# Performance work log

Hardware: AMD Instinct MI355X
Metric: run time of the kernel (lower is better)

The kernel has to match this reference:

```python
import jax, jax.numpy as jnp
import numpy as np

B, S, D = 2, 2048, 2048
NH, NKV, HD = 16, 4, 128  # num_heads, num_key_value_heads, head_dim

def setup_inputs() -> dict:
    key = jax.random.key(0)
    ks = jax.random.split(key, 5)
    sc = 0.02
    return {
        "hidden_states": jax.random.normal(ks[0], (B, S, D), jnp.float32),
        "Wq": jax.random.normal(ks[1], (NH * HD, D), jnp.float32) * sc,
        "Wk": jax.random.normal(ks[2], (NKV * HD, D), jnp.float32) * sc,
        "Wv": jax.random.normal(ks[3], (NKV * HD, D), jnp.float32) * sc,
        "Wo": jax.random.normal(ks[4], (D, NH * HD), jnp.float32) * sc,
    }

def reference(hidden_states, Wq, Wk, Wv, Wo):
    b, s, d = hidden_states.shape
    # projections (LLaMA linear: x @ W.T)
    q = jnp.einsum('bsd,ed->bse', hidden_states, Wq).reshape(b, s, NH, HD).transpose(0, 2, 1, 3)
    k = jnp.einsum('bsd,ed->bse', hidden_states, Wk).reshape(b, s, NKV, HD).transpose(0, 2, 1, 3)
    v = jnp.einsum('bsd,ed->bse', hidden_states, Wv).reshape(b, s, NKV, HD).transpose(0, 2, 1, 3)
    # GQA: repeat kv heads
    n_rep = NH // NKV
    k = jnp.repeat(k, n_rep, axis=1)  # [b, NH, s, HD]
    v = jnp.repeat(v, n_rep, axis=1)
    scale = 1.0 / jnp.sqrt(jnp.asarray(HD, hidden_states.dtype))
    scores = jnp.einsum('bhqd,bhkd->bhqk', q, k) * scale
    causal = jnp.tril(jnp.ones((s, s), bool))
    scores = jnp.where(causal, scores, jnp.asarray(-jnp.inf, scores.dtype))
    attn = jax.nn.softmax(scores, axis=-1)
    out = jnp.einsum('bhqk,bhkd->bhqd', attn, v)  # [b, NH, s, HD]
    out = out.transpose(0, 2, 1, 3).reshape(b, s, NH * HD)
    return jnp.einsum('bse,de->bsd', out, Wo)
```

## Files before the change

### kernel.cpp

```cpp
#include <hip/hip_runtime.h>

typedef unsigned short u16;
typedef unsigned int u32;
typedef __attribute__((ext_vector_type(4))) float f32x4;
typedef __attribute__((ext_vector_type(16))) float f32x16;
typedef __attribute__((ext_vector_type(8))) short bf16x8;


__device__ __forceinline__ u16 f2b(float f) {
  u32 u = __builtin_bit_cast(u32, f);
  u = (u + 0x7fffu + ((u >> 16) & 1u)) >> 16;
  return (u16)u;
}

__device__ __forceinline__ void gload_lds16(const void* g, void* l) {
  __builtin_amdgcn_global_load_lds((const __attribute__((address_space(1))) u32*)g,
                                   (__attribute__((address_space(3))) u32*)l, 16, 0, 0);
}

#if __has_builtin(__builtin_amdgcn_permlane32_swap)
#define HAS_PLS 1
__device__ __forceinline__ void pls(u32 x, u32 y, u32& rx, u32& ry) {
  auto r = __builtin_amdgcn_permlane32_swap(x, y, false, false);
  rx = (u32)r[0];
  ry = (u32)r[1];
}
#endif

__device__ __forceinline__ float xhalf_max(float v) {
#ifdef HAS_PLS
  u32 a, b;
  pls(__builtin_bit_cast(u32, v), __builtin_bit_cast(u32, v), a, b);
  return fmaxf(__builtin_bit_cast(float, a), __builtin_bit_cast(float, b));
#else
  return fmaxf(v, __shfl_xor(v, 32));
#endif
}

__device__ __forceinline__ float xhalf_sum(float v) {
#ifdef HAS_PLS
  u32 a, b;
  pls(__builtin_bit_cast(u32, v), __builtin_bit_cast(u32, v), a, b);
  return __builtin_bit_cast(float, a) + __builtin_bit_cast(float, b);
#else
  return v + __shfl_xor(v, 32);
#endif
}

__device__ __forceinline__ void xexchange(int hi, u32 a0, u32 a1, u32 a2, u32 a3, u32* o) {
#ifdef HAS_PLS
  pls(a0, a2, o[0], o[2]);
  pls(a1, a3, o[1], o[3]);
#else
  u32 xa0 = (u32)__shfl_xor((int)a0, 32), xa1 = (u32)__shfl_xor((int)a1, 32);
  u32 xa2 = (u32)__shfl_xor((int)a2, 32), xa3 = (u32)__shfl_xor((int)a3, 32);
  o[0] = hi ? xa2 : a0;
  o[1] = hi ? xa3 : a1;
  o[2] = hi ? a2 : xa0;
  o[3] = hi ? a3 : xa1;
#endif
}

__device__ __forceinline__ u32 pktrunc(float lo, float hif) {
  return (__builtin_bit_cast(u32, lo) >> 16) | (__builtin_bit_cast(u32, hif) & 0xffff0000u);
}

__global__ void cvt_bf16(const float* __restrict__ src, u16* __restrict__ dst, int n) {
  int stride = gridDim.x * blockDim.x * 4;
  for (int idx = (blockIdx.x * blockDim.x + threadIdx.x) * 4; idx < n; idx += stride) {
    float4 v = *(const float4*)(src + idx);
    ushort4 o;
    o.x = f2b(v.x); o.y = f2b(v.y); o.z = f2b(v.z); o.w = f2b(v.w);
    *(ushort4*)(dst + idx) = o;
  }
}

__global__ void cvt_w4(const float* __restrict__ Wq, const float* __restrict__ Wk,
                       const float* __restrict__ Wv, const float* __restrict__ Wo,
                       u16* __restrict__ dst) {
  const int total = 10485760;
  int stride = gridDim.x * blockDim.x * 4;
  for (int idx = (blockIdx.x * blockDim.x + threadIdx.x) * 4; idx < total; idx += stride) {
    const float* src;
    int off;
    if (idx < 4194304) { src = Wq; off = idx; }
    else if (idx < 5242880) { src = Wk; off = idx - 4194304; }
    else if (idx < 6291456) { src = Wv; off = idx - 5242880; }
    else { src = Wo; off = idx - 6291456; }
    float4 v = *(const float4*)(src + off);
    ushort4 o;
    o.x = f2b(v.x); o.y = f2b(v.y); o.z = f2b(v.z); o.w = f2b(v.w);
    *(ushort4*)(dst + idx) = o;
  }
}

template<int OUT_MODE>
__global__ __launch_bounds__(256) void gemm_bt(const u16* __restrict__ A, const u16* __restrict__ B,
                                               void* __restrict__ Cout, int M, int N, int Kd,
                                               u16* __restrict__ Kout, u16* __restrict__ Vtout) {
  __shared__ u16 smem[(OUT_MODE == 3) ? 16384 : 8192];
  u16* sA = smem;
  u16* sB = smem + 4096;
  const int tid = threadIdx.x;
  const int l = tid & 63, w = tid >> 6;
  const int wr = w >> 1, wc = w & 1;
  const int g = l >> 4, c = l & 15;
  const int tm = blockIdx.y * 128, tn = blockIdx.x * 128;

  f32x4 acc[4][4] = {};

  const int r0 = tid >> 2, cc = (tid & 3) << 3;

  for (int k0 = 0; k0 < Kd; k0 += 32) {
    __syncthreads();
    {
      const u16* srcA0 = A + (size_t)(tm + r0) * Kd + k0 + cc;
      const u16* srcB0 = B + (size_t)(tn + r0) * Kd + k0 + cc;
      gload_lds16(srcA0, (char*)sA + w * 1024);
      gload_lds16(srcB0, (char*)sB + w * 1024);
      gload_lds16(srcA0 + (size_t)64 * Kd, (char*)sA + 4096 + w * 1024);
      gload_lds16(srcB0 + (size_t)64 * Kd, (char*)sB + 4096 + w * 1024);
    }
    __syncthreads();

    bf16x8 af[4], bfr[4];
#pragma unroll
    for (int m = 0; m < 4; ++m)
      af[m] = *(const bf16x8*)(sA + (wr * 64 + m * 16 + c) * 32 + g * 8);
#pragma unroll
    for (int n = 0; n < 4; ++n)
      bfr[n] = *(const bf16x8*)(sB + (wc * 64 + n * 16 + c) * 32 + g * 8);
#pragma unroll
    for (int m = 0; m < 4; ++m)
#pragma unroll
      for (int n = 0; n < 4; ++n)
        acc[m][n] = __builtin_amdgcn_mfma_f32_16x16x32_bf16(af[m], bfr[n], acc[m][n], 0, 0, 0);
  }

  if constexpr (OUT_MODE == 3) {
    if (tn >= 2048) {
      const bool isK = tn < 2560;
      __syncthreads();
#pragma unroll
      for (int m = 0; m < 4; ++m)
#pragma unroll
        for (int n = 0; n < 4; ++n)
#pragma unroll
          for (int i = 0; i < 4; ++i) {
            int lr = wr * 64 + m * 16 + g * 4 + i;
            int lc = wc * 64 + n * 16 + c;
            int off;
            if (isK)
              off = ((lr >> 5) << 12) + ((lc >> 4) << 9) + (((lc >> 3) & 1) << 8) +
                    ((lr & 31) << 3) + (lc & 7);
            else
              off = ((lr >> 5) << 12) + (((lr >> 4) & 1) << 11) + ((lc >> 5) << 9) +
                    (((lr >> 3) & 1) << 8) + ((lc & 31) << 3) + (lr & 7);
            smem[off] = f2b(acc[m][n][i]);
          }
      __syncthreads();
      const int e0 = tn - (isK ? 2048 : 2560);
      const int bb = tm >> 11;
      u16* dstbase = (isK ? Kout : Vtout) +
                     ((((size_t)(bb * 4 + (e0 >> 7)) * 64 + ((tm & 2047) >> 5))) << 12);
#pragma unroll
      for (int ps = 0; ps < 8; ++ps) {
        int idx = ps * 2048 + tid * 8;
        *(bf16x8*)(dstbase + idx) = *(const bf16x8*)(smem + idx);
      }
      return;
    }
  }

#pragma unroll
  for (int m = 0; m < 4; ++m)
#pragma unroll
    for (int n = 0; n < 4; ++n)
#pragma unroll
      for (int i = 0; i < 4; ++i) {
        int row = tm + wr * 64 + m * 16 + g * 4 + i;
        int col = tn + wc * 64 + n * 16 + c;
        float v = acc[m][n][i];
        if constexpr (OUT_MODE == 2) {
          ((float*)Cout)[(size_t)row * N + col] = v;
        } else {
          ((u16*)Cout)[(size_t)row * 2048 + col] = f2b(v);
        }
      }
}

__global__ __launch_bounds__(256, 2) void attn_fwd(const u16* __restrict__ Q, const u16* __restrict__ Kf,
                                                   const u16* __restrict__ Vf, u16* __restrict__ AO) {
  const int l = threadIdx.x & 63, w = threadIdx.x >> 6;
  const int ql = l & 31, hi = l >> 5;
  const int bh = blockIdx.y;
  const int b = bh >> 4, h = bh & 15;
  const int kvh = h >> 2;

  __shared__ float4 mO[2][16][64];
  __shared__ float mML[2][2][64];

  const float sm = 0.08838834764831845f * 1.4426950408889634f;

  const u16* Kfb = Kf + (size_t)(b * 4 + kvh) * 64 * 4096 + l * 8;
  const u16* Vfb = Vf + (size_t)(b * 4 + kvh) * 64 * 4096 + l * 8;

  const int ti = w & 1, kvhalf = w >> 1;
  const int t = ti ? (63 - (int)blockIdx.x) : (int)blockIdx.x;
  const int q0 = t * 32;

  bf16x8 qf[8];
  {
    const u16* qb = Q + ((size_t)(b * 2048 + q0 + ql)) * 2048 + h * 128 + hi * 8;
#pragma unroll
    for (int ck = 0; ck < 8; ++ck) qf[ck] = *(const bf16x8*)(qb + ck * 16);
  }

  f32x16 acc[4] = {};
  float mrow = -1e30f, lrow = 0.f;

  bf16x8 kfa[8], kfb[8];

#define LOADK(KF, KV0)                                                        \
  do {                                                                        \
    const u16* kb_ = Kfb + (size_t)((KV0) >> 5) * 4096;                       \
    _Pragma("unroll") for (int ck = 0; ck < 8; ++ck)                          \
        KF[ck] = *(const bf16x8*)(kb_ + ck * 512);                            \
  } while (0)

#define COMPUTE(KF, KV0)                                                      \
  do {                                                                        \
    bf16x8 vtf[2][4];                                                         \
    {                                                                         \
      const u16* vb_ = Vfb + (size_t)((KV0) >> 5) * 4096;                     \
      _Pragma("unroll") for (int ks = 0; ks < 2; ++ks)                        \
      _Pragma("unroll") for (int db = 0; db < 4; ++db)                        \
          vtf[ks][db] = *(const bf16x8*)(vb_ + (ks * 4 + db) * 512);          \
    }                                                                         \
    f32x16 sacc = {};                                                         \
    __builtin_amdgcn_s_setprio(1);                                            \
    _Pragma("unroll") for (int ck = 0; ck < 8; ++ck)                          \
        sacc = __builtin_amdgcn_mfma_f32_32x32x16_bf16(KF[ck], qf[ck], sacc, 0, 0, 0); \
    __builtin_amdgcn_s_setprio(0);                                            \
    if ((KV0) == q0) {                             \
      _Pragma("unroll") for (int r = 0; r < 16; ++r) {                        \
        int crow = (r & 3) + 8 * (r >> 2) + 4 * hi;                           \
        if (crow > ql) sacc[r] = -1e30f;                                      \
      }                                                                       \
    }                                                                         \
    float t0 = fmaxf(sacc[0], sacc[1]), t1 = fmaxf(sacc[2], sacc[3]);         \
    float t2 = fmaxf(sacc[4], sacc[5]), t3 = fmaxf(sacc[6], sacc[7]);         \
    float t4 = fmaxf(sacc[8], sacc[9]), t5 = fmaxf(sacc[10], sacc[11]);       \
    float t6 = fmaxf(sacc[12], sacc[13]), t7 = fmaxf(sacc[14], sacc[15]);     \
    float mx = fmaxf(fmaxf(fmaxf(t0, t1), fmaxf(t2, t3)),                     \
                     fmaxf(fmaxf(t4, t5), fmaxf(t6, t7)));                    \
    mx = xhalf_max(mx);                                                       \
    float p[16];                                                              \
    _Pragma("unroll") for (int r = 0; r < 16; ++r)                            \
        p[r] = exp2f((sacc[r] - mrow) * sm);                                  \
    if (!__all((mx - mrow) * sm <= 8.0f)) {                \
      float mnew = fmaxf(mrow, mx);                                           \
      float rs = exp2f((mrow - mnew) * sm);                                   \
      mrow = mnew;                                                            \
      lrow *= rs;                                                             \
      _Pragma("unroll") for (int db = 0; db < 4; ++db)                        \
      _Pragma("unroll") for (int r = 0; r < 16; ++r) acc[db][r] *= rs;        \
      _Pragma("unroll") for (int r = 0; r < 16; ++r)                          \
          p[r] = exp2f((sacc[r] - mrow) * sm);                                \
    }                                                                         \
    float s0 = p[0] + p[1], s1 = p[2] + p[3], s2 = p[4] + p[5], s3 = p[6] + p[7]; \
    float s4 = p[8] + p[9], s5 = p[10] + p[11], s6 = p[12] + p[13], s7 = p[14] + p[15]; \
    float psum = ((s0 + s1) + (s2 + s3)) + ((s4 + s5) + (s6 + s7));           \
    lrow += xhalf_sum(psum);                                                  \
    u32 a0 = pktrunc(p[0], p[1]), a1 = pktrunc(p[2], p[3]);                   \
    u32 a2 = pktrunc(p[4], p[5]), a3 = pktrunc(p[6], p[7]);                   \
    u32 b0 = pktrunc(p[8], p[9]), b1 = pktrunc(p[10], p[11]);                 \
    u32 b2 = pktrunc(p[12], p[13]), b3 = pktrunc(p[14], p[15]);               \
    union { bf16x8 v; u32 u[4]; } pa0, pa1;                                   \
    xexchange(hi, a0, a1, a2, a3, pa0.u);                                     \
    xexchange(hi, b0, b1, b2, b3, pa1.u);                                     \
    __builtin_amdgcn_s_setprio(1);                                            \
    _Pragma("unroll") for (int db = 0; db < 4; ++db) {                        \
      acc[db] = __builtin_amdgcn_mfma_f32_32x32x16_bf16(vtf[0][db], pa0.v, acc[db], 0, 0, 0); \
      acc[db] = __builtin_amdgcn_mfma_f32_32x32x16_bf16(vtf[1][db], pa1.v, acc[db], 0, 0, 0); \
    }                                                                         \
    __builtin_amdgcn_s_setprio(0);                                            \
  } while (0)

  int kv0 = kvhalf * 32;
  if (kv0 <= q0) {
    LOADK(kfa, kv0);
    while (true) {
      bool more = kv0 + 64 <= q0;
      if (more) LOADK(kfb, kv0 + 64);
      COMPUTE(kfa, kv0);
      if (!more) break;
      kv0 += 64;
      more = kv0 + 64 <= q0;
      if (more) LOADK(kfa, kv0 + 64);
      COMPUTE(kfb, kv0);
      if (!more) break;
      kv0 += 64;
    }
  }
#undef LOADK
#undef COMPUTE

  if (kvhalf) {
#pragma unroll
    for (int db = 0; db < 4; ++db)
#pragma unroll
      for (int rq = 0; rq < 4; ++rq) {
        float4 v;
        v.x = acc[db][rq * 4 + 0];
        v.y = acc[db][rq * 4 + 1];
        v.z = acc[db][rq * 4 + 2];
        v.w = acc[db][rq * 4 + 3];
        mO[ti][db * 4 + rq][l] = v;
      }
    mML[ti][0][l] = mrow;
    mML[ti][1][l] = lrow;
  }
  __syncthreads();
  if (!kvhalf) {
    float m1 = mML[ti][0][l], l1 = mML[ti][1][l];
    float mnew = fmaxf(mrow, m1);
    float s0 = exp2f((mrow - mnew) * sm);
    float s1 = exp2f((m1 - mnew) * sm);
    float inv = 1.0f / (lrow * s0 + l1 * s1);
    float f0 = s0 * inv, f1 = s1 * inv;
    u16* ob = AO + (size_t)(b * 2048 + q0 + ql) * 2048 + h * 128 + hi * 4;
#pragma unroll
    for (int db = 0; db < 4; ++db)
#pragma unroll
      for (int rq = 0; rq < 4; ++rq) {
        float4 o1 = mO[ti][db * 4 + rq][l];
        ushort4 o;
        o.x = f2b(acc[db][rq * 4 + 0] * f0 + o1.x * f1);
        o.y = f2b(acc[db][rq * 4 + 1] * f0 + o1.y * f1);
        o.z = f2b(acc[db][rq * 4 + 2] * f0 + o1.z * f1);
        o.w = f2b(acc[db][rq * 4 + 3] * f0 + o1.w * f1);
        *(ushort4*)(ob + db * 32 + rq * 8) = o;
      }
  }
}

extern "C" void kernel_launch(void* const* d_in, const int* in_sizes, int n_in,
                              void* d_out, int out_size, void* d_ws, size_t ws_size,
                              hipStream_t stream) {
  const float* X = (const float*)d_in[0];
  const float* Wq = (const float*)d_in[1];
  const float* Wk = (const float*)d_in[2];
  const float* Wv = (const float*)d_in[3];
  const float* Wo = (const float*)d_in[4];

  u16* ws = (u16*)d_ws;
  const size_t nX = 8388608;
  const size_t nWq = 4194304;
  const size_t nWk = 1048576;
  u16* Xb = ws;
  u16* Wqb = Xb + nX;
  u16* Wkb = Wqb + nWq;
  u16* Wvb = Wkb + nWk;
  u16* Wob = Wvb + nWk;
  u16* Qb = Wob + nWq;
  u16* Kfb = Qb + nX;
  u16* Vfb = Kfb + 2097152;
  u16* AOb = Vfb + 2097152;
  if (ws_size < (size_t)(39845888) * 2) return;

  cvt_bf16<<<2048, 256, 0, stream>>>(X, Xb, (int)nX);
  cvt_w4<<<2048, 256, 0, stream>>>(Wq, Wk, Wv, Wo, Wqb);

  gemm_bt<3><<<dim3(24, 32), 256, 0, stream>>>(Xb, Wqb, Qb, 4096, 3072, 2048, Kfb, Vfb);

  attn_fwd<<<dim3(32, 32), 256, 0, stream>>>(Qb, Kfb, Vfb, AOb);

  gemm_bt<2><<<dim3(16, 32), 256, 0, stream>>>(AOb, Wob, d_out, 4096, 2048, 2048, nullptr, nullptr);
}
```

Before: 216.2 us.

## Split each query tile's KV range across four waves with tree merge

Each block now processes a single 32-row query tile, and its four waves stride over the KV range in steps of 128 instead of two waves handling paired mirrored tiles. Partial softmax states are combined through LDS in a two-step tree reduction, and the grid doubles with tiles launched heaviest-first. This shortens the per-wave serial KV loop and improves load balance. In exchange it adds extra barriers and merge work, and each block gets less work.

```diff
diff --git a/kernel.cpp b/kernel.cpp
--- a/kernel.cpp
+++ b/kernel.cpp
@@ -205,8 +205,7 @@
   const u16* Kfb = Kf + (size_t)(b * 4 + kvh) * 64 * 4096 + l * 8;
   const u16* Vfb = Vf + (size_t)(b * 4 + kvh) * 64 * 4096 + l * 8;
 
-  const int ti = w & 1, kvhalf = w >> 1;
-  const int t = ti ? (63 - (int)blockIdx.x) : (int)blockIdx.x;
+  const int t = 63 - (int)blockIdx.x;
   const int q0 = t * 32;
 
   bf16x8 qf[8];
@@ -287,62 +286,82 @@
     __builtin_amdgcn_s_setprio(0);                                            \
   } while (0)
 
-  int kv0 = kvhalf * 32;
+  int kv0 = w * 32;
   if (kv0 <= q0) {
     LOADK(kfa, kv0);
     while (true) {
-      bool more = kv0 + 64 <= q0;
-      if (more) LOADK(kfb, kv0 + 64);
+      bool more = kv0 + 128 <= q0;
+      if (more) LOADK(kfb, kv0 + 128);
       COMPUTE(kfa, kv0);
       if (!more) break;
-      kv0 += 64;
-      more = kv0 + 64 <= q0;
-      if (more) LOADK(kfa, kv0 + 64);
+      kv0 += 128;
+      more = kv0 + 128 <= q0;
+      if (more) LOADK(kfa, kv0 + 128);
       COMPUTE(kfb, kv0);
       if (!more) break;
-      kv0 += 64;
+      kv0 += 128;
     }
   }
 #undef LOADK
 #undef COMPUTE
 
-  if (kvhalf) {
+#define PUBLISH(SLOT)                                                         \
+  do {                                                                        \
+    _Pragma("unroll") for (int db = 0; db < 4; ++db)                          \
+    _Pragma("unroll") for (int rq = 0; rq < 4; ++rq) {                        \
+      float4 v;                                                               \
+      v.x = acc[db][rq * 4 + 0];                                              \
+      v.y = acc[db][rq * 4 + 1];                                              \
+      v.z = acc[db][rq * 4 + 2];                                              \
+      v.w = acc[db][rq * 4 + 3];                                              \
+      mO[SLOT][db * 4 + rq][l] = v;                                           \
+    }                                                                         \
+    mML[SLOT][0][l] = mrow;                                                   \
+    mML[SLOT][1][l] = lrow;                                                   \
+  } while (0)
+
+#define MERGE(SLOT)                                                           \
+  do {                                                                        \
+    float m1 = mML[SLOT][0][l], l1 = mML[SLOT][1][l];                         \
+    float mnew = fmaxf(mrow, m1);                                             \
+    float f0 = exp2f((mrow - mnew) * sm);                                     \
+    float f1 = exp2f((m1 - mnew) * sm);                                       \
+    mrow = mnew;                                                              \
+    lrow = lrow * f0 + l1 * f1;                                               \
+    _Pragma("unroll") for (int db = 0; db < 4; ++db)                          \
+    _Pragma("unroll") for (int rq = 0; rq < 4; ++rq) {                        \
+      float4 o1 = mO[SLOT][db * 4 + rq][l];                                   \
+      acc[db][rq * 4 + 0] = acc[db][rq * 4 + 0] * f0 + o1.x * f1;             \
+      acc[db][rq * 4 + 1] = acc[db][rq * 4 + 1] * f0 + o1.y * f1;             \
+      acc[db][rq * 4 + 2] = acc[db][rq * 4 + 2] * f0 + o1.z * f1;             \
+      acc[db][rq * 4 + 3] = acc[db][rq * 4 + 3] * f0 + o1.w * f1;             \
+    }                                                                         \
+  } while (0)
+
+  if (w >= 2) PUBLISH(w - 2);
+  __syncthreads();
+  if (w < 2) MERGE(w);
+  __syncthreads();
+  if (w == 1) PUBLISH(0);
+  __syncthreads();
+  if (w == 0) {
+    MERGE(0);
+    float inv = 1.0f / lrow;
+    u16* ob = AO + (size_t)(b * 2048 + q0 + ql) * 2048 + h * 128 + hi * 4;
 #pragma unroll
     for (int db = 0; db < 4; ++db)
 #pragma unroll
       for (int rq = 0; rq < 4; ++rq) {
-        float4 v;
-        v.x = acc[db][rq * 4 + 0];
-        v.y = acc[db][rq * 4 + 1];
-        v.z = acc[db][rq * 4 + 2];
-        v.w = acc[db][rq * 4 + 3];
-        mO[ti][db * 4 + rq][l] = v;
-      }
-    mML[ti][0][l] = mrow;
-    mML[ti][1][l] = lrow;
-  }
-  __syncthreads();
-  if (!kvhalf) {
-    float m1 = mML[ti][0][l], l1 = mML[ti][1][l];
-    float mnew = fmaxf(mrow, m1);
-    float s0 = exp2f((mrow - mnew) * sm);
-    float s1 = exp2f((m1 - mnew) * sm);
-    float inv = 1.0f / (lrow * s0 + l1 * s1);
-    float f0 = s0 * inv, f1 = s1 * inv;
-    u16* ob = AO + (size_t)(b * 2048 + q0 + ql) * 2048 + h * 128 + hi * 4;
-#pragma unroll
-    for (int db = 0; db < 4; ++db)
-#pragma unroll
-      for (int rq = 0; rq < 4; ++rq) {
-        float4 o1 = mO[ti][db * 4 + rq][l];
         ushort4 o;
-        o.x = f2b(acc[db][rq * 4 + 0] * f0 + o1.x * f1);
-        o.y = f2b(acc[db][rq * 4 + 1] * f0 + o1.y * f1);
-        o.z = f2b(acc[db][rq * 4 + 2] * f0 + o1.z * f1);
-        o.w = f2b(acc[db][rq * 4 + 3] * f0 + o1.w * f1);
+        o.x = f2b(acc[db][rq * 4 + 0] * inv);
+        o.y = f2b(acc[db][rq * 4 + 1] * inv);
+        o.z = f2b(acc[db][rq * 4 + 2] * inv);
+        o.w = f2b(acc[db][rq * 4 + 3] * inv);
         *(ushort4*)(ob + db * 32 + rq * 8) = o;
       }
   }
+#undef PUBLISH
+#undef MERGE
 }
 
 extern "C" void kernel_launch(void* const* d_in, const int* in_sizes, int n_in,
@@ -374,7 +393,7 @@
 
   gemm_bt<3><<<dim3(24, 32), 256, 0, stream>>>(Xb, Wqb, Qb, 4096, 3072, 2048, Kfb, Vfb);
 
-  attn_fwd<<<dim3(32, 32), 256, 0, stream>>>(Qb, Kfb, Vfb, AOb);
+  attn_fwd<<<dim3(64, 32), 256, 0, stream>>>(Qb, Kfb, Vfb, AOb);
 
   gemm_bt<2><<<dim3(16, 32), 256, 0, stream>>>(AOb, Wob, d_out, 4096, 2048, 2048, nullptr, nullptr);
 }
```

Result: slower. 232.6 us (+7.6%).
